# Performance work log

Hardware: AMD Instinct MI355X
Metric: run time of the kernel (lower is better)

## Reference

```python
import jax, jax.numpy as jnp
import numpy as np

EMBED = 1024
HEADS = 16
HEAD_DIM = EMBED // HEADS


def setup_inputs() -> dict:
    key = jax.random.key(0)
    ks = jax.random.split(key, 8)
    N, L = 4, 2048
    values = jax.random.normal(ks[0], (N, L, EMBED), dtype=jnp.float32)
    keys_ = jax.random.normal(ks[1], (N, L, EMBED), dtype=jnp.float32)
    queries = jax.random.normal(ks[2], (N, L, EMBED), dtype=jnp.float32)
    s = 1.0 / np.sqrt(HEAD_DIM)
    Wv = jax.random.normal(ks[3], (HEAD_DIM, HEAD_DIM), dtype=jnp.float32) * s
    Wk = jax.random.normal(ks[4], (HEAD_DIM, HEAD_DIM), dtype=jnp.float32) * s
    Wq = jax.random.normal(ks[5], (HEAD_DIM, HEAD_DIM), dtype=jnp.float32) * s
    Wo = jax.random.normal(ks[6], (EMBED, EMBED), dtype=jnp.float32) * (1.0 / np.sqrt(EMBED))
    bo = jnp.zeros((EMBED,), dtype=jnp.float32)
    return {"values": values, "keys": keys_, "queries": queries,
            "Wv": Wv, "Wk": Wk, "Wq": Wq, "Wo": Wo, "bo": bo}


def reference(values, keys, queries, Wv, Wk, Wq, Wo, bo):
    N, L, _ = queries.shape
    # split heads: [N, L, H, D]
    v = values.reshape(N, -1, HEADS, HEAD_DIM)
    k = keys.reshape(N, -1, HEADS, HEAD_DIM)
    q = queries.reshape(N, L, HEADS, HEAD_DIM)
    # per-head linear (same [D,D] weight shared across heads), torch Linear: x @ W.T
    v = jnp.einsum('nlhd,ed->nlhe', v, Wv)
    k = jnp.einsum('nlhd,ed->nlhe', k, Wk)
    q = jnp.einsum('nqhd,ed->nqhe', q, Wq)
    # attention scores [N, H, Q, K], scaled by sqrt(embed_size) as in source
    scores = jnp.einsum('nqhd,nkhd->nhqk', q, k) / jnp.sqrt(jnp.float32(EMBED))
    attn = jax.nn.softmax(scores, axis=-1)
    out = jnp.einsum('nhqk,nkhd->nqhd', attn, v).reshape(N, L, EMBED)
    return out @ Wo.T + bo
```

## Files before the change

### kernel.cpp

```cpp
#include <hip/hip_runtime.h>
#include <math.h>

#define EMBED 1024
#define HEADS 16
#define HD    64
#define NB    4
#define LSEQ  2048

typedef __attribute__((ext_vector_type(8))) short bf16x8;
typedef __attribute__((ext_vector_type(16))) float f32x16;

typedef __attribute__((address_space(1))) void as1_void;
typedef __attribute__((address_space(3))) void as3_void;

#if __has_builtin(__builtin_amdgcn_exp2f)
#define EXP2(x) __builtin_amdgcn_exp2f(x)
#else
#define EXP2(x) exp2f(x)
#endif

__device__ __forceinline__ void gload_lds16(const void* g, void* l) {
    __builtin_amdgcn_global_load_lds((const as1_void*)g, (as3_void*)l, 16, 0, 0);
}

__device__ inline bf16x8 as_bf16x8(uint4 u) {
    union { uint4 u; bf16x8 b; } c; c.u = u; return c.b;
}
__device__ inline unsigned short bf16r(float x) {
    unsigned u = __float_as_uint(x);
    u += 0x7fffu + ((u >> 16) & 1u);
    return (unsigned short)(u >> 16);
}
__device__ inline float bfh2f(unsigned short h) {
    return __uint_as_float(((unsigned)h) << 16);
}
__device__ inline void split2(float x, float y, unsigned& hw, unsigned& lw) {
    unsigned short hx = bf16r(x), hy = bf16r(y);
    unsigned short lx = bf16r(x - bfh2f(hx)), ly = bf16r(y - bfh2f(hy));
    hw = (unsigned)hx | ((unsigned)hy << 16);
    lw = (unsigned)lx | ((unsigned)ly << 16);
}

__global__ __launch_bounds__(256, 3) void proj_kernel(
    const float* __restrict__ Xv, const float* __restrict__ Xk, const float* __restrict__ Xq,
    const float* __restrict__ Wv, const float* __restrict__ Wk, const float* __restrict__ Wq,
    const float* __restrict__ Wo,
    unsigned short* __restrict__ Vt, unsigned short* __restrict__ Kp, unsigned short* __restrict__ Qp,
    unsigned short* __restrict__ Woh, unsigned short* __restrict__ Wol)
{
    __shared__ uint4 sXh[128 * 8];
    __shared__ uint4 sXl[128 * 8];
    __shared__ uint4 sWh[64 * 8];
    __shared__ uint4 sWl[64 * 8];

    const int t = threadIdx.x;

    if (blockIdx.z == 3) {
        int w_id = blockIdx.x + blockIdx.y * 64;
        int i = w_id * 256 + t;
        float4 v = ((const float4*)Wo)[i];
        ushort4 h4, l4;
        h4.x = bf16r(v.x); l4.x = bf16r(v.x - bfh2f(h4.x));
        h4.y = bf16r(v.y); l4.y = bf16r(v.y - bfh2f(h4.y));
        h4.z = bf16r(v.z); l4.z = bf16r(v.z - bfh2f(h4.z));
        h4.w = bf16r(v.w); l4.w = bf16r(v.w - bfh2f(h4.w));
        ((ushort4*)Woh)[i] = h4;
        ((ushort4*)Wol)[i] = l4;
        return;
    }

    const int lane = t & 63, w = t >> 6;
    const int l5 = lane & 31, hi = lane >> 5;
    const int h  = blockIdx.y;
    const int n  = blockIdx.x >> 4;
    const int l0 = (blockIdx.x & 15) * 128;
    const int p  = blockIdx.z;

    const float QSC = 1.44269504088896341f / 32.0f;
    const float* Xp = (p == 0) ? Xv : (p == 1) ? Xk : Xq;
    const float* Wp = (p == 0) ? Wv : (p == 1) ? Wk : Wq;

    const int frow = t >> 4;
    const int fcol = t & 15;

    {
        const float* xb = Xp + ((size_t)(n * LSEQ + l0 + frow)) * EMBED + h * HD + fcol * 4;
        unsigned short* dh = (unsigned short*)sXh;
        unsigned short* dl = (unsigned short*)sXl;
        #pragma unroll
        for (int i = 0; i < 8; ++i) {
            int row = frow + i * 16;
            float4 v = *(const float4*)(xb + (size_t)i * 16 * EMBED);
            int gg = fcol >> 1, s8 = (fcol & 1) * 4;
            int idx = row * 64 + ((gg ^ (row & 7)) * 8) + s8;
            uint2 hv, lv;
            split2(v.x, v.y, hv.x, lv.x);
            split2(v.z, v.w, hv.y, lv.y);
            *(uint2*)(dh + idx) = hv;
            *(uint2*)(dl + idx) = lv;
        }
    }
    #pragma unroll
    for (int i = 0; i < 2; ++i) {
        int u = t + 256 * i;
        int e = u >> 3, g = u & 7;
        const float* wb = Wp + u * 8;
        float4 v0 = *(const float4*)(wb);
        float4 v1 = *(const float4*)(wb + 4);
        uint4 hq, lq;
        split2(v0.x, v0.y, hq.x, lq.x);
        split2(v0.z, v0.w, hq.y, lq.y);
        split2(v1.x, v1.y, hq.z, lq.z);
        split2(v1.z, v1.w, hq.w, lq.w);
        int idx = e * 8 + (g ^ (e & 7));
        sWh[idx] = hq;
        sWl[idx] = lq;
    }
    __syncthreads();

    f32x16 acc0, acc1;
    #pragma unroll
    for (int i = 0; i < 16; ++i) { acc0[i] = 0.f; acc1[i] = 0.f; }

    const int xrow = w * 32 + l5;
    const int w0r = l5, w1r = 32 + l5;
    #pragma unroll
    for (int kc = 0; kc < 4; ++kc) {
        int gsel = kc * 2 + hi;
        bf16x8 xh = as_bf16x8(sXh[xrow * 8 + (gsel ^ (xrow & 7))]);
        bf16x8 xl = as_bf16x8(sXl[xrow * 8 + (gsel ^ (xrow & 7))]);
        bf16x8 wh0 = as_bf16x8(sWh[w0r * 8 + (gsel ^ (w0r & 7))]);
        bf16x8 wl0 = as_bf16x8(sWl[w0r * 8 + (gsel ^ (w0r & 7))]);
        bf16x8 wh1 = as_bf16x8(sWh[w1r * 8 + (gsel ^ (w1r & 7))]);
        bf16x8 wl1 = as_bf16x8(sWl[w1r * 8 + (gsel ^ (w1r & 7))]);
        if (p == 0) {
            acc0 = __builtin_amdgcn_mfma_f32_32x32x16_bf16(wh0, xh, acc0, 0, 0, 0);
            acc0 = __builtin_amdgcn_mfma_f32_32x32x16_bf16(wh0, xl, acc0, 0, 0, 0);
            acc0 = __builtin_amdgcn_mfma_f32_32x32x16_bf16(wl0, xh, acc0, 0, 0, 0);
            acc1 = __builtin_amdgcn_mfma_f32_32x32x16_bf16(wh1, xh, acc1, 0, 0, 0);
            acc1 = __builtin_amdgcn_mfma_f32_32x32x16_bf16(wh1, xl, acc1, 0, 0, 0);
            acc1 = __builtin_amdgcn_mfma_f32_32x32x16_bf16(wl1, xh, acc1, 0, 0, 0);
        } else {
            acc0 = __builtin_amdgcn_mfma_f32_32x32x16_bf16(xh, wh0, acc0, 0, 0, 0);
            acc0 = __builtin_amdgcn_mfma_f32_32x32x16_bf16(xh, wl0, acc0, 0, 0, 0);
            acc0 = __builtin_amdgcn_mfma_f32_32x32x16_bf16(xl, wh0, acc0, 0, 0, 0);
            acc1 = __builtin_amdgcn_mfma_f32_32x32x16_bf16(xh, wh1, acc1, 0, 0, 0);
            acc1 = __builtin_amdgcn_mfma_f32_32x32x16_bf16(xh, wl1, acc1, 0, 0, 0);
            acc1 = __builtin_amdgcn_mfma_f32_32x32x16_bf16(xl, wh1, acc1, 0, 0, 0);
        }
    }

    if (p == 0) {
        unsigned short* vb = Vt + (((size_t)(n * HEADS + h)) * HD) * LSEQ + l0 + w * 32 + l5;
        #pragma unroll
        for (int r = 0; r < 16; ++r) {
            int er = (r & 3) + 8 * (r >> 2) + 4 * hi;
            vb[(size_t)er * LSEQ]        = bf16r(acc0[r]);
            vb[(size_t)(32 + er) * LSEQ] = bf16r(acc1[r]);
        }
    } else {
        unsigned short* dst = (p == 1) ? Kp : Qp;
        float sc = (p == 2) ? QSC : 1.0f;
        unsigned short* db = dst + (((size_t)(n * HEADS + h)) * LSEQ + l0 + w * 32) * HD;
        #pragma unroll
        for (int r = 0; r < 16; ++r) {
            int tok = (r & 3) + 8 * (r >> 2) + 4 * hi;
            db[(size_t)tok * HD + l5]      = bf16r(acc0[r] * sc);
            db[(size_t)tok * HD + 32 + l5] = bf16r(acc1[r] * sc);
        }
    }
}

__global__ __launch_bounds__(256, 4) void attn_kernel(
    const unsigned short* __restrict__ Qp, const unsigned short* __restrict__ Kp,
    const unsigned short* __restrict__ Vt,
    unsigned short* __restrict__ AOh, unsigned short* __restrict__ AOl)
{
    __shared__ uint4 sK[2][64 * 8];
    __shared__ uint4 sV[2][64 * 8];

    const int t = threadIdx.x;
    const int lane = t & 63, w = t >> 6;
    const int l5 = lane & 31, hi = lane >> 5;

    const int b   = blockIdx.x + blockIdx.y * 16 + blockIdx.z * 256;
    const int xcd = b & 7, u = b >> 3;
    const int grp = xcd * 8 + (u >> 4);
    const int n   = grp >> 4, h = grp & 15;
    const int q0  = (u & 15) * 128;

    const size_t hoff = ((size_t)n * HEADS + h) * (size_t)(LSEQ * HD);
    const unsigned short* Kh = Kp + hoff;
    const unsigned short* Vh = Vt + hoff;

    bf16x8 qf[4];
    {
        const uint4* qg = (const uint4*)(Qp + hoff + (size_t)(q0 + w * 32 + l5) * HD);
        #pragma unroll
        for (int kc = 0; kc < 4; ++kc) qf[kc] = as_bf16x8(qg[kc * 2 + hi]);
    }

    f32x16 z16;
    #pragma unroll
    for (int i = 0; i < 16; ++i) z16[i] = 0.f;
    f32x16 Oa0 = z16, Oa1 = z16;
    float ls0 = 0.f, ls1 = 0.f;

    const int r0 = t >> 3;
    const int g0 = (t & 7) ^ (r0 & 7);
    const uint4* gK = (const uint4*)Kh;
    const uint4* gV = (const uint4*)Vh;

    #define STAGE(TILE, BUF)                                                        \
        do {                                                                        \
            int kb_ = (TILE) * 64;                                                  \
            gload_lds16(gK + (size_t)(kb_ + r0) * 8 + g0,        &sK[BUF][t]);      \
            gload_lds16(gK + (size_t)(kb_ + r0 + 32) * 8 + g0,   &sK[BUF][t + 256]);\
            gload_lds16(gV + (size_t)r0 * 256 + (kb_ >> 3) + g0, &sV[BUF][t]);      \
            gload_lds16(gV + (size_t)(r0 + 32) * 256 + (kb_ >> 3) + g0,             \
                        &sV[BUF][t + 256]);                                         \
        } while (0)

    #define COMPUTE(BUF)                                                            \
        do {                                                                        \
            _Pragma("unroll")                                                       \
            for (int tc = 0; tc < 2; ++tc) {                                        \
                int key = tc * 32 + l5;                                             \
                __builtin_amdgcn_s_setprio(1);                                      \
                bf16x8 kf0 = as_bf16x8(sK[BUF][key * 8 + (hi ^ (l5 & 7))]);         \
                f32x16 c = __builtin_amdgcn_mfma_f32_32x32x16_bf16(kf0, qf[0], z16, 0, 0, 0); \
                _Pragma("unroll")                                                   \
                for (int kc = 1; kc < 4; ++kc) {                                    \
                    bf16x8 kf = as_bf16x8(sK[BUF][key * 8 + ((kc * 2 + hi) ^ (l5 & 7))]); \
                    c = __builtin_amdgcn_mfma_f32_32x32x16_bf16(kf, qf[kc], c, 0, 0, 0);  \
                }                                                                   \
                __builtin_amdgcn_s_setprio(0);                                      \
                uint4 pwa, pwb;                                                     \
                {                                                                   \
                    float p0 = EXP2(c[0]),  p1 = EXP2(c[1]);                        \
                    float p2 = EXP2(c[2]),  p3 = EXP2(c[3]);                        \
                    ls0 += p0 + p1; ls1 += p2 + p3;                                 \
                    asm("v_cvt_pk_bf16_f32 %0, %1, %2" : "=v"(pwa.x) : "v"(p0), "v"(p1)); \
                    asm("v_cvt_pk_bf16_f32 %0, %1, %2" : "=v"(pwa.y) : "v"(p2), "v"(p3)); \
                    p0 = EXP2(c[4]);  p1 = EXP2(c[5]);                              \
                    p2 = EXP2(c[6]);  p3 = EXP2(c[7]);                              \
                    ls0 += p0 + p1; ls1 += p2 + p3;                                 \
                    asm("v_cvt_pk_bf16_f32 %0, %1, %2" : "=v"(pwa.z) : "v"(p0), "v"(p1)); \
                    asm("v_cvt_pk_bf16_f32 %0, %1, %2" : "=v"(pwa.w) : "v"(p2), "v"(p3)); \
                    p0 = EXP2(c[8]);  p1 = EXP2(c[9]);                              \
                    p2 = EXP2(c[10]); p3 = EXP2(c[11]);                             \
                    ls0 += p0 + p1; ls1 += p2 + p3;                                 \
                    asm("v_cvt_pk_bf16_f32 %0, %1, %2" : "=v"(pwb.x) : "v"(p0), "v"(p1)); \
                    asm("v_cvt_pk_bf16_f32 %0, %1, %2" : "=v"(pwb.y) : "v"(p2), "v"(p3)); \
                    p0 = EXP2(c[12]); p1 = EXP2(c[13]);                             \
                    p2 = EXP2(c[14]); p3 = EXP2(c[15]);                             \
                    ls0 += p0 + p1; ls1 += p2 + p3;                                 \
                    asm("v_cvt_pk_bf16_f32 %0, %1, %2" : "=v"(pwb.z) : "v"(p0), "v"(p1)); \
                    asm("v_cvt_pk_bf16_f32 %0, %1, %2" : "=v"(pwb.w) : "v"(p2), "v"(p3)); \
                }                                                                   \
                asm("v_permlane32_swap_b32 %0, %1" : "+v"(pwa.x), "+v"(pwa.z));     \
                asm("v_permlane32_swap_b32 %0, %1" : "+v"(pwa.y), "+v"(pwa.w));     \
                asm("v_permlane32_swap_b32 %0, %1" : "+v"(pwb.x), "+v"(pwb.z));     \
                asm("v_permlane32_swap_b32 %0, %1" : "+v"(pwb.y), "+v"(pwb.w));     \
                __builtin_amdgcn_s_setprio(1);                                      \
                {                                                                   \
                    int vg0 = tc * 4 + hi;                                          \
                    bf16x8 pa = as_bf16x8(pwa);                                     \
                    bf16x8 v0 = as_bf16x8(sV[BUF][ l5       * 8 + (vg0 ^ (l5 & 7))]); \
                    Oa0 = __builtin_amdgcn_mfma_f32_32x32x16_bf16(pa, v0, Oa0, 0, 0, 0); \
                    bf16x8 v1 = as_bf16x8(sV[BUF][(32 + l5) * 8 + (vg0 ^ (l5 & 7))]); \
                    Oa1 = __builtin_amdgcn_mfma_f32_32x32x16_bf16(pa, v1, Oa1, 0, 0, 0); \
                    int vg1 = tc * 4 + 2 + hi;                                      \
                    bf16x8 pb = as_bf16x8(pwb);                                     \
                    bf16x8 v2 = as_bf16x8(sV[BUF][ l5       * 8 + (vg1 ^ (l5 & 7))]); \
                    Oa0 = __builtin_amdgcn_mfma_f32_32x32x16_bf16(pb, v2, Oa0, 0, 0, 0); \
                    bf16x8 v3 = as_bf16x8(sV[BUF][(32 + l5) * 8 + (vg1 ^ (l5 & 7))]); \
                    Oa1 = __builtin_amdgcn_mfma_f32_32x32x16_bf16(pb, v3, Oa1, 0, 0, 0); \
                }                                                                   \
                __builtin_amdgcn_s_setprio(0);                                      \
            }                                                                       \
        } while (0)

    STAGE(0, 0);

    for (int tt = 0; tt < LSEQ / 64; tt += 2) {
        STAGE(tt + 1, 1);
        asm volatile("s_waitcnt vmcnt(4)" ::: "memory");
        __builtin_amdgcn_s_barrier();
        COMPUTE(0);
        __builtin_amdgcn_s_barrier();

        if (tt + 2 < LSEQ / 64) {
            STAGE(tt + 2, 0);
            asm volatile("s_waitcnt vmcnt(4)" ::: "memory");
        } else {
            asm volatile("s_waitcnt vmcnt(0)" ::: "memory");
        }
        __builtin_amdgcn_s_barrier();
        COMPUTE(1);
        __builtin_amdgcn_s_barrier();
    }
    #undef STAGE
    #undef COMPUTE

    float lsum = ls0 + ls1;
    lsum += __shfl_xor(lsum, 32);
    float inv = 1.0f / lsum;
    float* sLf = (float*)&sK[0][0];
    if (hi == 0) sLf[w * 32 + l5] = inv;
    __syncthreads();

    unsigned short* hB = AOh + hoff;
    unsigned short* lB = AOl + hoff;
    #pragma unroll
    for (int r = 0; r < 16; ++r) {
        int qr = (r & 3) + 8 * (r >> 2) + 4 * hi;
        float invq = sLf[w * 32 + qr];
        size_t row = (size_t)(q0 + w * 32 + qr) * HD;
        float o0 = Oa0[r] * invq;
        float o1 = Oa1[r] * invq;
        unsigned short h0 = bf16r(o0), h1 = bf16r(o1);
        hB[row +      l5] = h0;
        hB[row + 32 + l5] = h1;
        lB[row +      l5] = bf16r(o0 - bfh2f(h0));
        lB[row + 32 + l5] = bf16r(o1 - bfh2f(h1));
    }
}

__global__ __launch_bounds__(256, 3) void outproj_kernel(
    const unsigned short* __restrict__ AOh, const unsigned short* __restrict__ AOl,
    const unsigned short* __restrict__ Woh, const unsigned short* __restrict__ Wol,
    const float* __restrict__ bo, float* __restrict__ out)
{
    __shared__ uint4 sA[2][1024];
    __shared__ uint4 sB[2][512];

    const int t = threadIdx.x;
    const int lane = t & 63, w = t >> 6;
    const int l5 = lane & 31, hi = lane >> 5;

    const int bl  = blockIdx.x + blockIdx.y * 64;
    const int xcd = bl & 7, u = bl >> 3;
    const int m0  = (xcd * 8 + (u & 7)) * 128;
    const int e0  = (u >> 3) * 64;
    const int n   = m0 >> 11, l0 = m0 & 2047;

    #define SW(r) (((r) ^ ((r) >> 3)) & 7)

    #define OSTAGE(C, BUF)                                                            \
        do {                                                                          \
            int hh_ = (C) >> 1, hf_ = (C) & 1;                                        \
            const uint4* gAh_ = (const uint4*)(AOh) +                                 \
                (((size_t)n * HEADS + hh_) * LSEQ + l0) * 8 + hf_ * 4;                \
            const uint4* gAl_ = (const uint4*)(AOl) +                                 \
                (((size_t)n * HEADS + hh_) * LSEQ + l0) * 8 + hf_ * 4;                \
            const uint4* gBh_ = (const uint4*)(Woh) +                                 \
                (size_t)e0 * 128 + hh_ * 8 + hf_ * 4;                                 \
            const uint4* gBl_ = (const uint4*)(Wol) +                                 \
                (size_t)e0 * 128 + hh_ * 8 + hf_ * 4;                                 \
            _Pragma("unroll")                                                         \
            for (int i_ = 0; i_ < 4; ++i_) {                                          \
                int s_ = t + 256 * i_;                                                \
                int row_ = s_ >> 3, sg_ = (s_ & 7) ^ SW(row_);                        \
                const uint4* src_ = (sg_ < 4 ? gAh_ : gAl_) +                         \
                    (size_t)row_ * 8 + (sg_ & 3);                                     \
                gload_lds16(src_, &sA[BUF][s_]);                                      \
            }                                                                         \
            _Pragma("unroll")                                                         \
            for (int i_ = 0; i_ < 2; ++i_) {                                          \
                int s_ = t + 256 * i_;                                                \
                int row_ = s_ >> 3, sg_ = (s_ & 7) ^ SW(row_);                        \
                const uint4* src_ = (sg_ < 4 ? gBh_ : gBl_) +                         \
                    (size_t)row_ * 128 + (sg_ & 3);                                   \
                gload_lds16(src_, &sB[BUF][s_]);                                      \
            }                                                                         \
        } while (0)

    f32x16 acc0, acc1;
    #pragma unroll
    for (int i = 0; i < 16; ++i) { acc0[i] = 0.f; acc1[i] = 0.f; }

    OSTAGE(0, 0);
    int cur = 0;

    const int amr = w * 32 + l5;
    const int swa  = SW(amr);
    const int swb0 = SW(l5);
    const int swb1 = SW(32 + l5);

    for (int c = 0; c < 32; ++c) {
        if (c + 1 < 32) {
            OSTAGE(c + 1, cur ^ 1);
            asm volatile("s_waitcnt vmcnt(6)" ::: "memory");
        } else {
            asm volatile("s_waitcnt vmcnt(0)" ::: "memory");
        }
        __builtin_amdgcn_s_barrier();

        __builtin_amdgcn_s_setprio(1);
        #pragma unroll
        for (int ks = 0; ks < 2; ++ks) {
            int gx = ks * 2 + hi;
            bf16x8 ah  = as_bf16x8(sA[cur][amr * 8       + ( gx      ^ swa )]);
            bf16x8 al  = as_bf16x8(sA[cur][amr * 8       + ((gx + 4) ^ swa )]);
            bf16x8 bh0 = as_bf16x8(sB[cur][ l5       * 8 + ( gx      ^ swb0)]);
            bf16x8 bh1 = as_bf16x8(sB[cur][(32 + l5) * 8 + ( gx      ^ swb1)]);
            bf16x8 bl0 = as_bf16x8(sB[cur][ l5       * 8 + ((gx + 4) ^ swb0)]);
            bf16x8 bl1 = as_bf16x8(sB[cur][(32 + l5) * 8 + ((gx + 4) ^ swb1)]);

            acc0 = __builtin_amdgcn_mfma_f32_32x32x16_bf16(ah, bh0, acc0, 0, 0, 0);
            acc1 = __builtin_amdgcn_mfma_f32_32x32x16_bf16(ah, bh1, acc1, 0, 0, 0);
            acc0 = __builtin_amdgcn_mfma_f32_32x32x16_bf16(ah, bl0, acc0, 0, 0, 0);
            acc1 = __builtin_amdgcn_mfma_f32_32x32x16_bf16(ah, bl1, acc1, 0, 0, 0);
            acc0 = __builtin_amdgcn_mfma_f32_32x32x16_bf16(al, bh0, acc0, 0, 0, 0);
            acc1 = __builtin_amdgcn_mfma_f32_32x32x16_bf16(al, bh1, acc1, 0, 0, 0);
        }
        __builtin_amdgcn_s_setprio(0);
        __builtin_amdgcn_s_barrier();
        cur ^= 1;
    }
    #undef OSTAGE
    #undef SW

    float b0 = bo[e0 + l5];
    float b1 = bo[e0 + 32 + l5];
    #pragma unroll
    for (int r = 0; r < 16; ++r) {
        int row = m0 + w * 32 + (r & 3) + 8 * (r >> 2) + 4 * hi;
        float* o = out + (size_t)row * EMBED + e0;
        o[l5]      = acc0[r] + b0;
        o[32 + l5] = acc1[r] + b1;
    }
}

extern "C" void kernel_launch(void* const* d_in, const int* in_sizes, int n_in,
                              void* d_out, int out_size, void* d_ws, size_t ws_size,
                              hipStream_t stream)
{
    const float* values  = (const float*)d_in[0];
    const float* keys    = (const float*)d_in[1];
    const float* queries = (const float*)d_in[2];
    const float* Wv      = (const float*)d_in[3];
    const float* Wk      = (const float*)d_in[4];
    const float* Wq      = (const float*)d_in[5];
    const float* Wo      = (const float*)d_in[6];
    const float* bo      = (const float*)d_in[7];
    float* out = (float*)d_out;

    const size_t bufElems = (size_t)NB * HEADS * LSEQ * HD;
    unsigned short* Qp  = (unsigned short*)d_ws;
    unsigned short* Kp  = Qp  + bufElems;
    unsigned short* Vt  = Kp  + bufElems;
    unsigned short* AOh = Vt  + bufElems;
    unsigned short* AOl = AOh + bufElems;
    unsigned short* Woh = AOl + bufElems;
    unsigned short* Wol = Woh + (size_t)EMBED * EMBED;

    proj_kernel<<<dim3(NB * 16, HEADS, 4), 256, 0, stream>>>(
        values, keys, queries, Wv, Wk, Wq, Wo, Vt, Kp, Qp, Woh, Wol);
    attn_kernel<<<dim3(LSEQ / 128, HEADS, NB), 256, 0, stream>>>(Qp, Kp, Vt, AOh, AOl);
    outproj_kernel<<<dim3(NB * LSEQ / 128, EMBED / 64), 256, 0, stream>>>(AOh, AOl, Woh, Wol, bo, out);
}
```

Measured before the change: 318.6 us.

## Triple-buffer K/V tiles and interleave both QK chunks before softmax-PV

Moves the attention kernel's K/V LDS staging from double to triple buffering, so two tiles are in flight while one is computed. The loop becomes 10 unrolled triples plus a 2-tile epilogue. Inside each tile, both 32-key QK^T MFMA chains now run back to back, and V fragments are loaded before the exp/pack step, to raise MFMA-level parallelism and hide LDS latency. In exchange it uses more LDS and registers, and lowers launch bounds to 3 blocks per CU, which may reduce occupancy.

```diff
diff --git a/kernel.cpp b/kernel.cpp
--- a/kernel.cpp
+++ b/kernel.cpp
@@ -171,13 +171,13 @@
     }
 }
 
-__global__ __launch_bounds__(256, 4) void attn_kernel(
+__global__ __launch_bounds__(256, 3) void attn_kernel(
     const unsigned short* __restrict__ Qp, const unsigned short* __restrict__ Kp,
     const unsigned short* __restrict__ Vt,
     unsigned short* __restrict__ AOh, unsigned short* __restrict__ AOl)
 {
-    __shared__ uint4 sK[2][64 * 8];
-    __shared__ uint4 sV[2][64 * 8];
+    __shared__ uint4 sK[3][64 * 8];
+    __shared__ uint4 sV[3][64 * 8];
 
     const int t = threadIdx.x;
     const int lane = t & 63, w = t >> 6;
@@ -221,86 +221,119 @@
                         &sV[BUF][t + 256]);                                         \
         } while (0)
 
+    #define EXPPACK(C, PWA, PWB)                                                    \
+        do {                                                                        \
+            float p0 = EXP2(C[0]),  p1 = EXP2(C[1]);                                \
+            float p2 = EXP2(C[2]),  p3 = EXP2(C[3]);                                \
+            ls0 += p0 + p1; ls1 += p2 + p3;                                         \
+            asm("v_cvt_pk_bf16_f32 %0, %1, %2" : "=v"(PWA.x) : "v"(p0), "v"(p1));   \
+            asm("v_cvt_pk_bf16_f32 %0, %1, %2" : "=v"(PWA.y) : "v"(p2), "v"(p3));   \
+            p0 = EXP2(C[4]);  p1 = EXP2(C[5]);                                      \
+            p2 = EXP2(C[6]);  p3 = EXP2(C[7]);                                      \
+            ls0 += p0 + p1; ls1 += p2 + p3;                                         \
+            asm("v_cvt_pk_bf16_f32 %0, %1, %2" : "=v"(PWA.z) : "v"(p0), "v"(p1));   \
+            asm("v_cvt_pk_bf16_f32 %0, %1, %2" : "=v"(PWA.w) : "v"(p2), "v"(p3));   \
+            p0 = EXP2(C[8]);  p1 = EXP2(C[9]);                                      \
+            p2 = EXP2(C[10]); p3 = EXP2(C[11]);                                     \
+            ls0 += p0 + p1; ls1 += p2 + p3;                                         \
+            asm("v_cvt_pk_bf16_f32 %0, %1, %2" : "=v"(PWB.x) : "v"(p0), "v"(p1));   \
+            asm("v_cvt_pk_bf16_f32 %0, %1, %2" : "=v"(PWB.y) : "v"(p2), "v"(p3));   \
+            p0 = EXP2(C[12]); p1 = EXP2(C[13]);                                     \
+            p2 = EXP2(C[14]); p3 = EXP2(C[15]);                                     \
+            ls0 += p0 + p1; ls1 += p2 + p3;                                         \
+            asm("v_cvt_pk_bf16_f32 %0, %1, %2" : "=v"(PWB.z) : "v"(p0), "v"(p1));   \
+            asm("v_cvt_pk_bf16_f32 %0, %1, %2" : "=v"(PWB.w) : "v"(p2), "v"(p3));   \
+            asm("v_permlane32_swap_b32 %0, %1" : "+v"(PWA.x), "+v"(PWA.z));         \
+            asm("v_permlane32_swap_b32 %0, %1" : "+v"(PWA.y), "+v"(PWA.w));         \
+            asm("v_permlane32_swap_b32 %0, %1" : "+v"(PWB.x), "+v"(PWB.z));         \
+            asm("v_permlane32_swap_b32 %0, %1" : "+v"(PWB.y), "+v"(PWB.w));         \
+        } while (0)
+
     #define COMPUTE(BUF)                                                            \
         do {                                                                        \
-            _Pragma("unroll")                                                       \
-            for (int tc = 0; tc < 2; ++tc) {                                        \
-                int key = tc * 32 + l5;                                             \
-                __builtin_amdgcn_s_setprio(1);                                      \
-                bf16x8 kf0 = as_bf16x8(sK[BUF][key * 8 + (hi ^ (l5 & 7))]);         \
-                f32x16 c = __builtin_amdgcn_mfma_f32_32x32x16_bf16(kf0, qf[0], z16, 0, 0, 0); \
+            f32x16 c0, c1;                                                          \
+            __builtin_amdgcn_s_setprio(1);                                          \
+            {                                                                       \
+                bf16x8 ka = as_bf16x8(sK[BUF][ l5       * 8 + (hi ^ (l5 & 7))]);    \
+                bf16x8 kb = as_bf16x8(sK[BUF][(32 + l5) * 8 + (hi ^ (l5 & 7))]);    \
+                c0 = __builtin_amdgcn_mfma_f32_32x32x16_bf16(ka, qf[0], z16, 0, 0, 0); \
+                c1 = __builtin_amdgcn_mfma_f32_32x32x16_bf16(kb, qf[0], z16, 0, 0, 0); \
                 _Pragma("unroll")                                                   \
                 for (int kc = 1; kc < 4; ++kc) {                                    \
-                    bf16x8 kf = as_bf16x8(sK[BUF][key * 8 + ((kc * 2 + hi) ^ (l5 & 7))]); \
-                    c = __builtin_amdgcn_mfma_f32_32x32x16_bf16(kf, qf[kc], c, 0, 0, 0);  \
+                    bf16x8 k0 = as_bf16x8(sK[BUF][ l5       * 8 + ((kc * 2 + hi) ^ (l5 & 7))]); \
+                    bf16x8 k1 = as_bf16x8(sK[BUF][(32 + l5) * 8 + ((kc * 2 + hi) ^ (l5 & 7))]); \
+                    c0 = __builtin_amdgcn_mfma_f32_32x32x16_bf16(k0, qf[kc], c0, 0, 0, 0); \
+                    c1 = __builtin_amdgcn_mfma_f32_32x32x16_bf16(k1, qf[kc], c1, 0, 0, 0); \
                 }                                                                   \
-                __builtin_amdgcn_s_setprio(0);                                      \
-                uint4 pwa, pwb;                                                     \
-                {                                                                   \
-                    float p0 = EXP2(c[0]),  p1 = EXP2(c[1]);                        \
-                    float p2 = EXP2(c[2]),  p3 = EXP2(c[3]);                        \
-                    ls0 += p0 + p1; ls1 += p2 + p3;                                 \
-                    asm("v_cvt_pk_bf16_f32 %0, %1, %2" : "=v"(pwa.x) : "v"(p0), "v"(p1)); \
-                    asm("v_cvt_pk_bf16_f32 %0, %1, %2" : "=v"(pwa.y) : "v"(p2), "v"(p3)); \
-                    p0 = EXP2(c[4]);  p1 = EXP2(c[5]);                              \
-                    p2 = EXP2(c[6]);  p3 = EXP2(c[7]);                              \
-                    ls0 += p0 + p1; ls1 += p2 + p3;                                 \
-                    asm("v_cvt_pk_bf16_f32 %0, %1, %2" : "=v"(pwa.z) : "v"(p0), "v"(p1)); \
-                    asm("v_cvt_pk_bf16_f32 %0, %1, %2" : "=v"(pwa.w) : "v"(p2), "v"(p3)); \
-                    p0 = EXP2(c[8]);  p1 = EXP2(c[9]);                              \
-                    p2 = EXP2(c[10]); p3 = EXP2(c[11]);                             \
-                    ls0 += p0 + p1; ls1 += p2 + p3;                                 \
-                    asm("v_cvt_pk_bf16_f32 %0, %1, %2" : "=v"(pwb.x) : "v"(p0), "v"(p1)); \
-                    asm("v_cvt_pk_bf16_f32 %0, %1, %2" : "=v"(pwb.y) : "v"(p2), "v"(p3)); \
-                    p0 = EXP2(c[12]); p1 = EXP2(c[13]);                             \
-                    p2 = EXP2(c[14]); p3 = EXP2(c[15]);                             \
-                    ls0 += p0 + p1; ls1 += p2 + p3;                                 \
-                    asm("v_cvt_pk_bf16_f32 %0, %1, %2" : "=v"(pwb.z) : "v"(p0), "v"(p1)); \
-                    asm("v_cvt_pk_bf16_f32 %0, %1, %2" : "=v"(pwb.w) : "v"(p2), "v"(p3)); \
-                }                                                                   \
-                asm("v_permlane32_swap_b32 %0, %1" : "+v"(pwa.x), "+v"(pwa.z));     \
-                asm("v_permlane32_swap_b32 %0, %1" : "+v"(pwa.y), "+v"(pwa.w));     \
-                asm("v_permlane32_swap_b32 %0, %1" : "+v"(pwb.x), "+v"(pwb.z));     \
-                asm("v_permlane32_swap_b32 %0, %1" : "+v"(pwb.y), "+v"(pwb.w));     \
-                __builtin_amdgcn_s_setprio(1);                                      \
-                {                                                                   \
-                    int vg0 = tc * 4 + hi;                                          \
-                    bf16x8 pa = as_bf16x8(pwa);                                     \
-                    bf16x8 v0 = as_bf16x8(sV[BUF][ l5       * 8 + (vg0 ^ (l5 & 7))]); \
-                    Oa0 = __builtin_amdgcn_mfma_f32_32x32x16_bf16(pa, v0, Oa0, 0, 0, 0); \
-                    bf16x8 v1 = as_bf16x8(sV[BUF][(32 + l5) * 8 + (vg0 ^ (l5 & 7))]); \
-                    Oa1 = __builtin_amdgcn_mfma_f32_32x32x16_bf16(pa, v1, Oa1, 0, 0, 0); \
-                    int vg1 = tc * 4 + 2 + hi;                                      \
-                    bf16x8 pb = as_bf16x8(pwb);                                     \
-                    bf16x8 v2 = as_bf16x8(sV[BUF][ l5       * 8 + (vg1 ^ (l5 & 7))]); \
-                    Oa0 = __builtin_amdgcn_mfma_f32_32x32x16_bf16(pb, v2, Oa0, 0, 0, 0); \
-                    bf16x8 v3 = as_bf16x8(sV[BUF][(32 + l5) * 8 + (vg1 ^ (l5 & 7))]); \
-                    Oa1 = __builtin_amdgcn_mfma_f32_32x32x16_bf16(pb, v3, Oa1, 0, 0, 0); \
-                }                                                                   \
-                __builtin_amdgcn_s_setprio(0);                                      \
             }                                                                       \
+            __builtin_amdgcn_s_setprio(0);                                          \
+            uint4 pwa, pwb;                                                         \
+            bf16x8 v0, v1, v2, v3;                                                  \
+            v0 = as_bf16x8(sV[BUF][ l5       * 8 + ((0 + hi) ^ (l5 & 7))]);         \
+            v1 = as_bf16x8(sV[BUF][(32 + l5) * 8 + ((0 + hi) ^ (l5 & 7))]);         \
+            v2 = as_bf16x8(sV[BUF][ l5       * 8 + ((2 + hi) ^ (l5 & 7))]);         \
+            v3 = as_bf16x8(sV[BUF][(32 + l5) * 8 + ((2 + hi) ^ (l5 & 7))]);         \
+            EXPPACK(c0, pwa, pwb);                                                  \
+            __builtin_amdgcn_s_setprio(1);                                          \
+            {                                                                       \
+                bf16x8 pa = as_bf16x8(pwa), pb = as_bf16x8(pwb);                    \
+                Oa0 = __builtin_amdgcn_mfma_f32_32x32x16_bf16(pa, v0, Oa0, 0, 0, 0);\
+                Oa1 = __builtin_amdgcn_mfma_f32_32x32x16_bf16(pa, v1, Oa1, 0, 0, 0);\
+                Oa0 = __builtin_amdgcn_mfma_f32_32x32x16_bf16(pb, v2, Oa0, 0, 0, 0);\
+                Oa1 = __builtin_amdgcn_mfma_f32_32x32x16_bf16(pb, v3, Oa1, 0, 0, 0);\
+            }                                                                       \
+            __builtin_amdgcn_s_setprio(0);                                          \
+            v0 = as_bf16x8(sV[BUF][ l5       * 8 + ((4 + hi) ^ (l5 & 7))]);         \
+            v1 = as_bf16x8(sV[BUF][(32 + l5) * 8 + ((4 + hi) ^ (l5 & 7))]);         \
+            v2 = as_bf16x8(sV[BUF][ l5       * 8 + ((6 + hi) ^ (l5 & 7))]);         \
+            v3 = as_bf16x8(sV[BUF][(32 + l5) * 8 + ((6 + hi) ^ (l5 & 7))]);         \
+            EXPPACK(c1, pwa, pwb);                                                  \
+            __builtin_amdgcn_s_setprio(1);                                          \
+            {                                                                       \
+                bf16x8 pa = as_bf16x8(pwa), pb = as_bf16x8(pwb);                    \
+                Oa0 = __builtin_amdgcn_mfma_f32_32x32x16_bf16(pa, v0, Oa0, 0, 0, 0);\
+                Oa1 = __builtin_amdgcn_mfma_f32_32x32x16_bf16(pa, v1, Oa1, 0, 0, 0);\
+                Oa0 = __builtin_amdgcn_mfma_f32_32x32x16_bf16(pb, v2, Oa0, 0, 0, 0);\
+                Oa1 = __builtin_amdgcn_mfma_f32_32x32x16_bf16(pb, v3, Oa1, 0, 0, 0);\
+            }                                                                       \
+            __builtin_amdgcn_s_setprio(0);                                          \
         } while (0)
 
     STAGE(0, 0);
-
-    for (int tt = 0; tt < LSEQ / 64; tt += 2) {
-        STAGE(tt + 1, 1);
-        asm volatile("s_waitcnt vmcnt(4)" ::: "memory");
+    STAGE(1, 1);
+
+    #pragma unroll 1
+    for (int jj = 0; jj < 10; ++jj) {
+        int j = jj * 3;
+        STAGE(j + 2, 2);
+        asm volatile("s_waitcnt vmcnt(8)" ::: "memory");
         __builtin_amdgcn_s_barrier();
         COMPUTE(0);
         __builtin_amdgcn_s_barrier();
 
-        if (tt + 2 < LSEQ / 64) {
-            STAGE(tt + 2, 0);
-            asm volatile("s_waitcnt vmcnt(4)" ::: "memory");
-        } else {
-            asm volatile("s_waitcnt vmcnt(0)" ::: "memory");
-        }
+        STAGE(j + 3, 0);
+        asm volatile("s_waitcnt vmcnt(8)" ::: "memory");
         __builtin_amdgcn_s_barrier();
         COMPUTE(1);
         __builtin_amdgcn_s_barrier();
-    }
+
+        STAGE(j + 4, 1);
+        asm volatile("s_waitcnt vmcnt(8)" ::: "memory");
+        __builtin_amdgcn_s_barrier();
+        COMPUTE(2);
+        __builtin_amdgcn_s_barrier();
+    }
+    asm volatile("s_waitcnt vmcnt(4)" ::: "memory");
+    __builtin_amdgcn_s_barrier();
+    COMPUTE(0);
+    __builtin_amdgcn_s_barrier();
+    asm volatile("s_waitcnt vmcnt(0)" ::: "memory");
+    __builtin_amdgcn_s_barrier();
+    COMPUTE(1);
+    __builtin_amdgcn_s_barrier();
+
     #undef STAGE
+    #undef EXPPACK
     #undef COMPUTE
 
     float lsum = ls0 + ls1;
```

Measured after the change: 351.6 us. +10.4%, slower.

## Load out-projection A operand directly to registers, staging only weights in LDS

Applied to the files above, without the earlier changes.

The out-projection kernel stops staging the attention-output tile in LDS. Each lane now loads its own A fragments (hi and lo bf16 halves) from global memory straight into registers, double-buffered across even and odd chunks. Only the Wo tile stays in LDS, which cuts shared memory per block and allows raising launch bounds occupancy from 3 to 4. The trade-off is more per-lane global loads with less coalescing, extra register pressure, and vmcnt waits that must now count the register loads correctly.

```diff
diff --git a/kernel.cpp b/kernel.cpp
--- a/kernel.cpp
+++ b/kernel.cpp
@@ -327,12 +327,11 @@
     }
 }
 
-__global__ __launch_bounds__(256, 3) void outproj_kernel(
+__global__ __launch_bounds__(256, 4) void outproj_kernel(
     const unsigned short* __restrict__ AOh, const unsigned short* __restrict__ AOl,
     const unsigned short* __restrict__ Woh, const unsigned short* __restrict__ Wol,
     const float* __restrict__ bo, float* __restrict__ out)
 {
-    __shared__ uint4 sA[2][1024];
     __shared__ uint4 sB[2][512];
 
     const int t = threadIdx.x;
@@ -347,25 +346,13 @@
 
     #define SW(r) (((r) ^ ((r) >> 3)) & 7)
 
-    #define OSTAGE(C, BUF)                                                            \
+    #define BSTAGE(C, BUF)                                                            \
         do {                                                                          \
             int hh_ = (C) >> 1, hf_ = (C) & 1;                                        \
-            const uint4* gAh_ = (const uint4*)(AOh) +                                 \
-                (((size_t)n * HEADS + hh_) * LSEQ + l0) * 8 + hf_ * 4;                \
-            const uint4* gAl_ = (const uint4*)(AOl) +                                 \
-                (((size_t)n * HEADS + hh_) * LSEQ + l0) * 8 + hf_ * 4;                \
             const uint4* gBh_ = (const uint4*)(Woh) +                                 \
                 (size_t)e0 * 128 + hh_ * 8 + hf_ * 4;                                 \
             const uint4* gBl_ = (const uint4*)(Wol) +                                 \
                 (size_t)e0 * 128 + hh_ * 8 + hf_ * 4;                                 \
-            _Pragma("unroll")                                                         \
-            for (int i_ = 0; i_ < 4; ++i_) {                                          \
-                int s_ = t + 256 * i_;                                                \
-                int row_ = s_ >> 3, sg_ = (s_ & 7) ^ SW(row_);                        \
-                const uint4* src_ = (sg_ < 4 ? gAh_ : gAl_) +                         \
-                    (size_t)row_ * 8 + (sg_ & 3);                                     \
-                gload_lds16(src_, &sA[BUF][s_]);                                      \
-            }                                                                         \
             _Pragma("unroll")                                                         \
             for (int i_ = 0; i_ < 2; ++i_) {                                          \
                 int s_ = t + 256 * i_;                                                \
@@ -376,50 +363,77 @@
             }                                                                         \
         } while (0)
 
-    f32x16 acc0, acc1;
-    #pragma unroll
-    for (int i = 0; i < 16; ++i) { acc0[i] = 0.f; acc1[i] = 0.f; }
-
-    OSTAGE(0, 0);
-    int cur = 0;
-
     const int amr = w * 32 + l5;
-    const int swa  = SW(amr);
+    const size_t aRow = ((size_t)n * HEADS) * LSEQ * 8 + (size_t)(l0 + amr) * 8;
+    const uint4* pAh = (const uint4*)AOh + aRow;
+    const uint4* pAl = (const uint4*)AOl + aRow;
+    #define ALOAD(C, H0, H1, L0, L1)                                                  \
+        do {                                                                          \
+            size_t off_ = (size_t)((C) >> 1) * (LSEQ * 8) + ((C) & 1) * 4 + hi;       \
+            H0 = as_bf16x8(pAh[off_]);                                                \
+            H1 = as_bf16x8(pAh[off_ + 2]);                                            \
+            L0 = as_bf16x8(pAl[off_]);                                                \
+            L1 = as_bf16x8(pAl[off_ + 2]);                                            \
+        } while (0)
+
     const int swb0 = SW(l5);
     const int swb1 = SW(32 + l5);
 
-    for (int c = 0; c < 32; ++c) {
-        if (c + 1 < 32) {
-            OSTAGE(c + 1, cur ^ 1);
+    #define OCOMPUTE(BUF, H0, H1, L0, L1)                                             \
+        do {                                                                          \
+            __builtin_amdgcn_s_setprio(1);                                            \
+            _Pragma("unroll")                                                         \
+            for (int ks = 0; ks < 2; ++ks) {                                          \
+                int gx = ks * 2 + hi;                                                 \
+                bf16x8 ah = ks ? H1 : H0;                                             \
+                bf16x8 al = ks ? L1 : L0;                                             \
+                bf16x8 bh0 = as_bf16x8(sB[BUF][ l5       * 8 + ( gx      ^ swb0)]);   \
+                bf16x8 bh1 = as_bf16x8(sB[BUF][(32 + l5) * 8 + ( gx      ^ swb1)]);   \
+                bf16x8 bl0 = as_bf16x8(sB[BUF][ l5       * 8 + ((gx + 4) ^ swb0)]);   \
+                bf16x8 bl1 = as_bf16x8(sB[BUF][(32 + l5) * 8 + ((gx + 4) ^ swb1)]);   \
+                acc0 = __builtin_amdgcn_mfma_f32_32x32x16_bf16(ah, bh0, acc0, 0, 0, 0); \
+                acc1 = __builtin_amdgcn_mfma_f32_32x32x16_bf16(ah, bh1, acc1, 0, 0, 0); \
+                acc0 = __builtin_amdgcn_mfma_f32_32x32x16_bf16(ah, bl0, acc0, 0, 0, 0); \
+                acc1 = __builtin_amdgcn_mfma_f32_32x32x16_bf16(ah, bl1, acc1, 0, 0, 0); \
+                acc0 = __builtin_amdgcn_mfma_f32_32x32x16_bf16(al, bh0, acc0, 0, 0, 0); \
+                acc1 = __builtin_amdgcn_mfma_f32_32x32x16_bf16(al, bh1, acc1, 0, 0, 0); \
+            }                                                                         \
+            __builtin_amdgcn_s_setprio(0);                                            \
+        } while (0)
+
+    f32x16 acc0, acc1;
+    #pragma unroll
+    for (int i = 0; i < 16; ++i) { acc0[i] = 0.f; acc1[i] = 0.f; }
+
+    bf16x8 eH0, eH1, eL0, eL1;
+    bf16x8 oH0, oH1, oL0, oL1;
+
+    BSTAGE(0, 0);
+    ALOAD(0, eH0, eH1, eL0, eL1);
+
+    #pragma unroll 1
+    for (int c = 0; c < 32; c += 2) {
+        BSTAGE(c + 1, 1);
+        ALOAD(c + 1, oH0, oH1, oL0, oL1);
+        asm volatile("s_waitcnt vmcnt(6)" ::: "memory");
+        __builtin_amdgcn_s_barrier();
+        OCOMPUTE(0, eH0, eH1, eL0, eL1);
+        __builtin_amdgcn_s_barrier();
+
+        if (c + 2 < 32) {
+            BSTAGE(c + 2, 0);
+            ALOAD(c + 2, eH0, eH1, eL0, eL1);
             asm volatile("s_waitcnt vmcnt(6)" ::: "memory");
         } else {
             asm volatile("s_waitcnt vmcnt(0)" ::: "memory");
         }
         __builtin_amdgcn_s_barrier();
-
-        __builtin_amdgcn_s_setprio(1);
-        #pragma unroll
-        for (int ks = 0; ks < 2; ++ks) {
-            int gx = ks * 2 + hi;
-            bf16x8 ah  = as_bf16x8(sA[cur][amr * 8       + ( gx      ^ swa )]);
-            bf16x8 al  = as_bf16x8(sA[cur][amr * 8       + ((gx + 4) ^ swa )]);
-            bf16x8 bh0 = as_bf16x8(sB[cur][ l5       * 8 + ( gx      ^ swb0)]);
-            bf16x8 bh1 = as_bf16x8(sB[cur][(32 + l5) * 8 + ( gx      ^ swb1)]);
-            bf16x8 bl0 = as_bf16x8(sB[cur][ l5       * 8 + ((gx + 4) ^ swb0)]);
-            bf16x8 bl1 = as_bf16x8(sB[cur][(32 + l5) * 8 + ((gx + 4) ^ swb1)]);
-
-            acc0 = __builtin_amdgcn_mfma_f32_32x32x16_bf16(ah, bh0, acc0, 0, 0, 0);
-            acc1 = __builtin_amdgcn_mfma_f32_32x32x16_bf16(ah, bh1, acc1, 0, 0, 0);
-            acc0 = __builtin_amdgcn_mfma_f32_32x32x16_bf16(ah, bl0, acc0, 0, 0, 0);
-            acc1 = __builtin_amdgcn_mfma_f32_32x32x16_bf16(ah, bl1, acc1, 0, 0, 0);
-            acc0 = __builtin_amdgcn_mfma_f32_32x32x16_bf16(al, bh0, acc0, 0, 0, 0);
-            acc1 = __builtin_amdgcn_mfma_f32_32x32x16_bf16(al, bh1, acc1, 0, 0, 0);
-        }
-        __builtin_amdgcn_s_setprio(0);
-        __builtin_amdgcn_s_barrier();
-        cur ^= 1;
-    }
-    #undef OSTAGE
+        OCOMPUTE(1, oH0, oH1, oL0, oL1);
+        __builtin_amdgcn_s_barrier();
+    }
+    #undef BSTAGE
+    #undef ALOAD
+    #undef OCOMPUTE
     #undef SW
 
     float b0 = bo[e0 + l5];
```

Result: slower. 329.6 us (+3.5%).
